# Kernel optimization log

Hardware: AMD Instinct MI355X
Metric: run time of the kernel (lower is better)

## Reference

```python
import jax, jax.numpy as jnp
import numpy as np

# module hyperparameters (from init_kwargs): kernel_size=(KH,KW), stride_size=(SH,SW)
KH, KW = 8, 8
SH, SW = 4, 4


def setup_inputs() -> dict:
    key = jax.random.key(0)
    x = jax.random.normal(key, (8, 64, 96, 96), dtype=jnp.float32)
    return {"x": x}


def _local_autocorr(x):
    """Local window self-correlation.

    For each kH x kW window (extracted with stride (SH,SW)), compute the
    correlation of the window with itself shifted by every offset
    (dy - KH//2, dx - KW//2), dy in [0,KH), dx in [0,KW), zero-padded
    outside the window. Output: [B, C, nH, nW, KH, KW].
    """
    B, C, H, W = x.shape
    nH = (H - KH) // SH + 1
    nW = (W - KW) // SW + 1
    # window gather indices
    ys = (jnp.arange(nH) * SH)[:, None] + jnp.arange(KH)[None, :]  # [nH, KH]
    xs = (jnp.arange(nW) * SW)[:, None] + jnp.arange(KW)[None, :]  # [nW, KW]
    # [B, C, nH, KH, nW, KW] -> [N, KH, KW], N = B*C*nH*nW
    patches = x[:, :, ys[:, :, None, None], xs[None, None, :, :]]
    patches = patches.transpose(0, 1, 2, 4, 3, 5).reshape(-1, KH, KW)
    N = patches.shape[0]
    # zero-pad each window so every shift stays in-bounds
    pt, pb = KH // 2, KH - 1 - KH // 2
    pl, pr = KW // 2, KW - 1 - KW // 2
    padded = jnp.pad(patches, ((0, 0), (pt, pb), (pl, pr)))  # [N, 2KH-1, 2KW-1]
    # depthwise (per-window) cross-correlation: out[n, dy, dx] =
    #   sum_{y,x} padded[n, dy + y, dx + x] * patches[n, y, x]
    out = jax.lax.conv_general_dilated(
        padded[None],           # [1, N, 2KH-1, 2KW-1]
        patches[:, None],       # [N, 1, KH, KW]
        window_strides=(1, 1),
        padding='VALID',
        dimension_numbers=('NCHW', 'OIHW', 'NCHW'),
        feature_group_count=N,
    )[0]                        # [N, KH, KW]
    return out.reshape(B, C, nH, nW, KH, KW)


def reference(x):
    return _local_autocorr(x)
```

## Files before the change

kernel.cpp:

```cpp
#include <hip/hip_runtime.h>


constexpr int KH = 8, KW = 8, SH = 4, SW = 4;
constexpr int B = 8, C = 64, H = 96, W = 96;
constexpr int nH = (H - KH) / SH + 1;
constexpr int nW = (W - KW) / SW + 1;
constexpr int NWIN = B * C * nH * nW;
constexpr int TPB = 64;
constexpr int HALFW = 32;
constexpr int OSTRIDE = 65;

__global__ __launch_bounds__(TPB, 2) void
local_autocorr_kernel(const float* __restrict__ x, float* __restrict__ out) {
    __shared__ float lds[HALFW * OSTRIDE];

    const int tid = threadIdx.x;
    const int n = blockIdx.x * TPB + tid;

    const int w  = n % nW;
    const int tt = n / nW;
    const int h  = tt % nH;
    const int bc = tt / nH;

    const float* xp = x + ((size_t)bc * H + (size_t)h * SH) * W + (size_t)w * SW;

    float accA[3][8];
    float c50 = 0.f, c60 = 0.f, c70 = 0.f;
#pragma unroll
    for (int k = 0; k < 3; ++k)
#pragma unroll
        for (int dx = 0; dx < 8; ++dx) accA[k][dx] = 0.f;

    {
        float rows[8][8];
        {
            const float4 lo = *reinterpret_cast<const float4*>(xp);
            const float4 hi = *reinterpret_cast<const float4*>(xp + 4);
            rows[0][0]=lo.x; rows[0][1]=lo.y; rows[0][2]=lo.z; rows[0][3]=lo.w;
            rows[0][4]=hi.x; rows[0][5]=hi.y; rows[0][6]=hi.z; rows[0][7]=hi.w;
        }
#pragma unroll
        for (int r = 0; r < 8; ++r) {
            if (r < 7) {
                const float4 lo = *reinterpret_cast<const float4*>(xp + (size_t)(r+1)*W);
                const float4 hi = *reinterpret_cast<const float4*>(xp + (size_t)(r+1)*W + 4);
                rows[r+1][0]=lo.x; rows[r+1][1]=lo.y; rows[r+1][2]=lo.z; rows[r+1][3]=lo.w;
                rows[r+1][4]=hi.x; rows[r+1][5]=hi.y; rows[r+1][6]=hi.z; rows[r+1][7]=hi.w;
            }
#pragma unroll
            for (int d = 0; d <= 2; ++d) {
                if (d > r) continue;
#pragma unroll
                for (int dx = 0; dx < 8; ++dx) {
                    const int OX = dx - 4;
#pragma unroll
                    for (int j = 0; j < 8; ++j) {
                        if (j + OX < 0 || j + OX >= 8) continue;
                        accA[d][dx] = fmaf(rows[r-d][j+OX], rows[r][j], accA[d][dx]);
                    }
                }
                if (d == 1) {
                    c50 = fmaf(rows[r][0], rows[r-1][4], c50);
                    c50 = fmaf(rows[r][1], rows[r-1][5], c50);
                    c50 = fmaf(rows[r][2], rows[r-1][6], c50);
                    c50 = fmaf(rows[r][3], rows[r-1][7], c50);
                } else if (d == 2) {
                    c60 = fmaf(rows[r][0], rows[r-2][4], c60);
                    c60 = fmaf(rows[r][1], rows[r-2][5], c60);
                    c60 = fmaf(rows[r][2], rows[r-2][6], c60);
                    c60 = fmaf(rows[r][3], rows[r-2][7], c60);
                }
            }
            __builtin_amdgcn_sched_barrier(0);
        }
    }

    asm volatile("" ::: "memory");

    float accB[2][8];
#pragma unroll
    for (int k = 0; k < 2; ++k)
#pragma unroll
        for (int dx = 0; dx < 8; ++dx) accB[k][dx] = 0.f;

    {
        float rows[8][8];
#pragma unroll
        for (int k = 0; k < 4; ++k) {
            const float4 lo = *reinterpret_cast<const float4*>(xp + (size_t)k*W);
            const float4 hi = *reinterpret_cast<const float4*>(xp + (size_t)k*W + 4);
            rows[k][0]=lo.x; rows[k][1]=lo.y; rows[k][2]=lo.z; rows[k][3]=lo.w;
            rows[k][4]=hi.x; rows[k][5]=hi.y; rows[k][6]=hi.z; rows[k][7]=hi.w;
        }
#pragma unroll
        for (int r = 3; r < 8; ++r) {
            if (r < 7) {
                const float4 lo = *reinterpret_cast<const float4*>(xp + (size_t)(r+1)*W);
                const float4 hi = *reinterpret_cast<const float4*>(xp + (size_t)(r+1)*W + 4);
                rows[r+1][0]=lo.x; rows[r+1][1]=lo.y; rows[r+1][2]=lo.z; rows[r+1][3]=lo.w;
                rows[r+1][4]=hi.x; rows[r+1][5]=hi.y; rows[r+1][6]=hi.z; rows[r+1][7]=hi.w;
            }
#pragma unroll
            for (int d = 3; d <= 4; ++d) {
                if (d > r) continue;
#pragma unroll
                for (int dx = 0; dx < 8; ++dx) {
                    const int OX = dx - 4;
#pragma unroll
                    for (int j = 0; j < 8; ++j) {
                        if (j + OX < 0 || j + OX >= 8) continue;
                        accB[d-3][dx] = fmaf(rows[r-d][j+OX], rows[r][j], accB[d-3][dx]);
                    }
                }
                if (d == 3) {
                    c70 = fmaf(rows[r][0], rows[r-3][4], c70);
                    c70 = fmaf(rows[r][1], rows[r-3][5], c70);
                    c70 = fmaf(rows[r][2], rows[r-3][6], c70);
                    c70 = fmaf(rows[r][3], rows[r-3][7], c70);
                }
            }
            __builtin_amdgcn_sched_barrier(0);
        }
    }

    float* obase = out + (size_t)blockIdx.x * TPB * 64;
#pragma unroll
    for (int ph = 0; ph < 2; ++ph) {
        if ((tid >> 5) == ph) {
            float* slot = &lds[(tid & 31) * OSTRIDE];
            *reinterpret_cast<float4*>(slot + 0)  = make_float4(accB[1][0], accB[1][1], accB[1][2], accB[1][3]);
            *reinterpret_cast<float4*>(slot + 4)  = make_float4(accB[1][4], accB[1][5], accB[1][6], accB[1][7]);
            *reinterpret_cast<float4*>(slot + 8)  = make_float4(accB[0][0], accB[0][1], accB[0][2], accB[0][3]);
            *reinterpret_cast<float4*>(slot + 12) = make_float4(accB[0][4], accB[0][5], accB[0][6], accB[0][7]);
            *reinterpret_cast<float4*>(slot + 16) = make_float4(accA[2][0], accA[2][1], accA[2][2], accA[2][3]);
            *reinterpret_cast<float4*>(slot + 20) = make_float4(accA[2][4], accA[2][5], accA[2][6], accA[2][7]);
            *reinterpret_cast<float4*>(slot + 24) = make_float4(accA[1][0], accA[1][1], accA[1][2], accA[1][3]);
            *reinterpret_cast<float4*>(slot + 28) = make_float4(accA[1][4], accA[1][5], accA[1][6], accA[1][7]);
            *reinterpret_cast<float4*>(slot + 32) = make_float4(accA[0][0], accA[0][1], accA[0][2], accA[0][3]);
            *reinterpret_cast<float4*>(slot + 36) = make_float4(accA[0][4], accA[0][5], accA[0][6], accA[0][7]);
            *reinterpret_cast<float4*>(slot + 40) = make_float4(c50,        accA[1][7], accA[1][6], accA[1][5]);
            *reinterpret_cast<float4*>(slot + 44) = make_float4(accA[1][4], accA[1][3], accA[1][2], accA[1][1]);
            *reinterpret_cast<float4*>(slot + 48) = make_float4(c60,        accA[2][7], accA[2][6], accA[2][5]);
            *reinterpret_cast<float4*>(slot + 52) = make_float4(accA[2][4], accA[2][3], accA[2][2], accA[2][1]);
            *reinterpret_cast<float4*>(slot + 56) = make_float4(c70,        accB[0][7], accB[0][6], accB[0][5]);
            *reinterpret_cast<float4*>(slot + 60) = make_float4(accB[0][4], accB[0][3], accB[0][2], accB[0][1]);
        }
        __syncthreads();
#pragma unroll
        for (int k = 0; k < 8; ++k) {
            const int flat4 = tid + k * 64;
            const float4 v = *reinterpret_cast<const float4*>(
                &lds[(flat4 >> 4) * OSTRIDE + (flat4 & 15) * 4]);
            *reinterpret_cast<float4*>(obase + (size_t)ph * HALFW * 64 + flat4 * 4) = v;
        }
        __syncthreads();
    }
}

extern "C" void kernel_launch(void* const* d_in, const int* in_sizes, int n_in,
                              void* d_out, int out_size, void* d_ws, size_t ws_size,
                              hipStream_t stream) {
    const float* x = (const float*)d_in[0];
    float* out = (float*)d_out;

    const int blocks = NWIN / TPB;
    local_autocorr_kernel<<<blocks, TPB, 0, stream>>>(x, out);
}
```

Baseline: 31.38 us.

## Remap blocks per XCD for L2 locality and prefetch rows two ahead

Block IDs are remapped so that each XCD (assuming 8 XCDs with round-robin dispatch) handles a contiguous range of windows. Overlapping input rows shared by neighbouring windows should then hit in that XCD's own L2 instead of spreading across all of them. Row loads are also issued two rows ahead of their use rather than one, which hides more global-load latency. The deeper prefetch keeps more rows live in registers and may raise register pressure under the launch bounds.

New measurement: 29.86 us. 4.8% less time.

```diff
diff --git a/kernel.cpp b/kernel.cpp
--- a/kernel.cpp
+++ b/kernel.cpp
@@ -9,13 +9,18 @@
 constexpr int TPB = 64;
 constexpr int HALFW = 32;
 constexpr int OSTRIDE = 65;
+constexpr int NBLK = NWIN / TPB;
+constexpr int NXCD = 8;
+constexpr int CPX = NBLK / NXCD;
 
 __global__ __launch_bounds__(TPB, 2) void
 local_autocorr_kernel(const float* __restrict__ x, float* __restrict__ out) {
     __shared__ float lds[HALFW * OSTRIDE];
 
     const int tid = threadIdx.x;
-    const int n = blockIdx.x * TPB + tid;
+    const int bid = (int)blockIdx.x;
+    const int blk = (bid % NXCD) * CPX + bid / NXCD;
+    const int n = blk * TPB + tid;
 
     const int w  = n % nW;
     const int tt = n / nW;
@@ -31,22 +36,21 @@
 #pragma unroll
         for (int dx = 0; dx < 8; ++dx) accA[k][dx] = 0.f;
 
+#define LOADROW(dst, ri)                                                        \
+    {                                                                           \
+        const float4 lo_ = *reinterpret_cast<const float4*>(xp + (size_t)(ri)*W);     \
+        const float4 hi_ = *reinterpret_cast<const float4*>(xp + (size_t)(ri)*W + 4); \
+        dst[0]=lo_.x; dst[1]=lo_.y; dst[2]=lo_.z; dst[3]=lo_.w;                 \
+        dst[4]=hi_.x; dst[5]=hi_.y; dst[6]=hi_.z; dst[7]=hi_.w;                 \
+    }
+
     {
         float rows[8][8];
-        {
-            const float4 lo = *reinterpret_cast<const float4*>(xp);
-            const float4 hi = *reinterpret_cast<const float4*>(xp + 4);
-            rows[0][0]=lo.x; rows[0][1]=lo.y; rows[0][2]=lo.z; rows[0][3]=lo.w;
-            rows[0][4]=hi.x; rows[0][5]=hi.y; rows[0][6]=hi.z; rows[0][7]=hi.w;
-        }
+        LOADROW(rows[0], 0)
+        LOADROW(rows[1], 1)
 #pragma unroll
         for (int r = 0; r < 8; ++r) {
-            if (r < 7) {
-                const float4 lo = *reinterpret_cast<const float4*>(xp + (size_t)(r+1)*W);
-                const float4 hi = *reinterpret_cast<const float4*>(xp + (size_t)(r+1)*W + 4);
-                rows[r+1][0]=lo.x; rows[r+1][1]=lo.y; rows[r+1][2]=lo.z; rows[r+1][3]=lo.w;
-                rows[r+1][4]=hi.x; rows[r+1][5]=hi.y; rows[r+1][6]=hi.z; rows[r+1][7]=hi.w;
-            }
+            if (r < 6) LOADROW(rows[r + 2], r + 2)
 #pragma unroll
             for (int d = 0; d <= 2; ++d) {
                 if (d > r) continue;
@@ -86,20 +90,10 @@
     {
         float rows[8][8];
 #pragma unroll
-        for (int k = 0; k < 4; ++k) {
-            const float4 lo = *reinterpret_cast<const float4*>(xp + (size_t)k*W);
-            const float4 hi = *reinterpret_cast<const float4*>(xp + (size_t)k*W + 4);
-            rows[k][0]=lo.x; rows[k][1]=lo.y; rows[k][2]=lo.z; rows[k][3]=lo.w;
-            rows[k][4]=hi.x; rows[k][5]=hi.y; rows[k][6]=hi.z; rows[k][7]=hi.w;
-        }
+        for (int k = 0; k < 5; ++k) LOADROW(rows[k], k)
 #pragma unroll
         for (int r = 3; r < 8; ++r) {
-            if (r < 7) {
-                const float4 lo = *reinterpret_cast<const float4*>(xp + (size_t)(r+1)*W);
-                const float4 hi = *reinterpret_cast<const float4*>(xp + (size_t)(r+1)*W + 4);
-                rows[r+1][0]=lo.x; rows[r+1][1]=lo.y; rows[r+1][2]=lo.z; rows[r+1][3]=lo.w;
-                rows[r+1][4]=hi.x; rows[r+1][5]=hi.y; rows[r+1][6]=hi.z; rows[r+1][7]=hi.w;
-            }
+            if (r < 6) LOADROW(rows[r + 2], r + 2)
 #pragma unroll
             for (int d = 3; d <= 4; ++d) {
                 if (d > r) continue;
@@ -122,8 +116,9 @@
             __builtin_amdgcn_sched_barrier(0);
         }
     }
+#undef LOADROW
 
-    float* obase = out + (size_t)blockIdx.x * TPB * 64;
+    float* obase = out + (size_t)blk * TPB * 64;
 #pragma unroll
     for (int ph = 0; ph < 2; ++ph) {
         if ((tid >> 5) == ph) {
@@ -163,6 +158,5 @@
     const float* x = (const float*)d_in[0];
     float* out = (float*)d_out;
 
-    const int blocks = NWIN / TPB;
-    local_autocorr_kernel<<<blocks, TPB, 0, stream>>>(x, out);
+    local_autocorr_kernel<<<NBLK, TPB, 0, stream>>>(x, out);
 }
```
